# Kernel tuning notes

Hardware: AMD Instinct MI355X
Metric: run time of the kernel (lower is better)

Reference implementation:

```python
import jax, jax.numpy as jnp
import numpy as np

B, T, C = 1, 2048, 2048
H, N = 16, 128            # num_attention_heads, head_size
KVH = 4                   # num_key_value_heads
N_REP = H // KVH
D_DECAY, D_AAA, D_MV, D_MK, D_GATE = 160, 96, 64, 64, 160
ROPE_THETA = 1000000.0
EPS = 1e-6

def _rms_norm(h, w):
    var = jnp.mean(jnp.square(h.astype(jnp.float32)), axis=-1, keepdims=True)
    return (w * (h.astype(jnp.float32) * jax.lax.rsqrt(var + EPS))).astype(h.dtype)

def _rotate_half(q):
    q1, q2 = jnp.split(q, 2, axis=-1)
    return jnp.concatenate([-q2, q1], axis=-1)

def setup_inputs():
    key = jax.random.key(0)
    ks = jax.random.split(key, 24)
    f = jnp.float32
    rn = lambda k, shape, s=1.0: jax.random.normal(k, shape, dtype=f) * s
    half = N // 2
    inv_freq = 1.0 / (ROPE_THETA ** (jnp.arange(half, dtype=f) / half))
    freqs = jnp.arange(T, dtype=f)[:, None] * inv_freq[None, :]
    emb = jnp.concatenate([freqs, freqs], axis=-1)
    return {
        "x": rn(ks[0], (B, T, C)),
        "v_first": rn(ks[1], (B, T, KVH, N)),
        "k_first": rn(ks[2], (B, T, KVH, N)),
        "attention_mask": jnp.ones((B, T), f),
        "cos": jnp.cos(emb)[None],
        "sin": jnp.sin(emb)[None],
        "w0": rn(ks[3], (1, 1, H * N), 0.5) - 2.0,
        "w1": rn(ks[4], (C, D_DECAY), 0.02),
        "w2": rn(ks[5], (D_DECAY, H * N), 0.02),
        "a0": rn(ks[6], (1, 1, H * N), 0.1),
        "a1": rn(ks[7], (C, D_AAA), 0.02),
        "a2": rn(ks[8], (D_AAA, H * N), 0.02),
        "v0": rn(ks[9], (1, 1, KVH * N), 0.1) + 0.73,
        "v1": rn(ks[10], (C, D_MV), 0.02),
        "v2": rn(ks[11], (D_MV, KVH * N), 0.02),
        "k0": rn(ks[12], (1, 1, KVH * N), 0.1) + 0.73,
        "k1": rn(ks[13], (C, D_MK), 0.02),
        "k2": rn(ks[14], (D_MK, KVH * N), 0.02),
        "g1": rn(ks[15], (C, D_GATE), 0.02),
        "g2": rn(ks[16], (D_GATE, H * N), 0.02),
        "r_k": rn(ks[17], (H, N), 0.02) - 0.04,
        "r_norm_w": jnp.ones((N,), f),
        "k_norm_w": jnp.ones((N,), f),
        "W_r": rn(ks[18], (C, H * N), 0.02),
        "W_k": rn(ks[19], (C, KVH * N), 0.02),
        "W_v": rn(ks[20], (C, KVH * N), 0.02),
        "W_o": rn(ks[21], (H * N, C), 0.02),
    }

def _forward(x, v_first, k_first, attention_mask, cos, sin, w0, w1, w2, a0, a1, a2,
             v0, v1, v2, k0, k1, k2, g1, g2, r_k, r_norm_w, k_norm_w, W_r, W_k, W_v, W_o):
    xm = x * attention_mask[..., None]
    r = _rms_norm((xm @ W_r).reshape(B, T, H, N), r_norm_w)
    k = _rms_norm((xm @ W_k).reshape(B, T, KVH, N), k_norm_w)
    v = (xm @ W_v).reshape(B, T, KVH, N)
    c, s = cos[:, :, None, :], sin[:, :, None, :]   # rope, unsqueeze_dim=2
    r = r * c + _rotate_half(r) * s
    k = k * c + _rotate_half(k) * s
    w = -jax.nn.softplus(-(w0 + jnp.tanh(xm @ w1) @ w2)) - 0.5   # (B,T,H*N), always <= -0.5
    a = jax.nn.sigmoid(a0 + (xm @ a1) @ a2).reshape(B, T, H, N)  # in-context learning rate
    g = jax.nn.sigmoid(xm @ g1) @ g2                             # output gate (B,T,H*N)
    # residual mixing with first-layer value/key (layer_id > 0 branch)
    v = v + (v_first - v) * jax.nn.sigmoid(v0 + (xm @ v1) @ v2).reshape(B, T, KVH, N)
    k = k + (k_first - k) * jax.nn.sigmoid(k0 + (xm @ k1) @ k2).reshape(B, T, KVH, N)
    k = jnp.repeat(k, N_REP, axis=2)   # GQA repeat_kv -> (B,T,H,N)
    v = jnp.repeat(v, N_REP, axis=2)
    kk = k / jnp.maximum(jnp.linalg.norm(k, axis=-1, keepdims=True), 1e-12)  # F.normalize
    aa, bb = -kk, kk * a               # rank-1 state-update vectors
    wdec = jnp.exp(-jnp.exp(w.reshape(B, T, H, N)))  # per-channel decay in (0,1)

    def step(S, xs):                   # RWKV-7 state recurrence; S: (B,H,N,N) value x key
        wt, rt, kt, vt, at, bt = xs    # each (B,H,N)
        sa = jnp.einsum('bhij,bhj->bhi', S, at)
        S = S * wt[:, :, None, :] + sa[..., None] * bt[:, :, None, :] + vt[..., None] * kt[:, :, None, :]
        return S, jnp.einsum('bhij,bhj->bhi', S, rt)

    S0 = jnp.zeros((B, H, N, N), jnp.float32)
    xs = tuple(jnp.moveaxis(t, 1, 0) for t in (wdec, r, k, v, aa, bb))  # time-major
    _, y = jax.lax.scan(step, S0, xs)
    y = jnp.moveaxis(y, 0, 1)          # (B,T,H,N)
    y = y + jnp.sum(r * k * r_k, axis=-1, keepdims=True) * v   # r_k bonus term
    return (y.reshape(B, T, H * N) * g) @ W_o

def reference(x, v_first, k_first, attention_mask, cos, sin, w0, w1, w2, a0, a1, a2,
              v0, v1, v2, k0, k1, k2, g1, g2, r_k, r_norm_w, k_norm_w, W_r, W_k, W_v, W_o):
    return _forward(x, v_first, k_first, attention_mask, cos, sin, w0, w1, w2, a0, a1, a2,
                    v0, v1, v2, k0, k1, k2, g1, g2, r_k, r_norm_w, k_norm_w, W_r, W_k, W_v, W_o)
```

## Files before the change

### kernel.cpp

```cpp
#include <hip/hip_runtime.h>
#include <hip/hip_bf16.h>
#include <math.h>

#define T_   2048
#define C_   2048
#define H_   16
#define N_   128
#define KVH_ 4

typedef __bf16 bf16x8 __attribute__((ext_vector_type(8)));
typedef __bf16 bf16x4 __attribute__((ext_vector_type(4)));
typedef float  f32x4  __attribute__((ext_vector_type(4)));

#define MFMA16(a, b, c) __builtin_amdgcn_mfma_f32_16x16x32_bf16(a, b, c, 0, 0, 0)

static __device__ __forceinline__ void gll16(const __bf16* g, __bf16* l) {
    __builtin_amdgcn_global_load_lds((const __attribute__((address_space(1))) void*)g,
                                     (__attribute__((address_space(3))) void*)l, 16, 0, 0);
}

static __device__ __forceinline__ float wave_sum_shfl(float v) {
#pragma unroll
    for (int m = 32; m >= 1; m >>= 1) v += __shfl_xor(v, m, 64);
    return v;
}
static __device__ __forceinline__ float block_sum_128(float v, float* sh2) {
    v = wave_sum_shfl(v);
    if ((threadIdx.x & 63) == 0) sh2[threadIdx.x >> 6] = v;
    __syncthreads();
    float r = sh2[0] + sh2[1];
    __syncthreads();
    return r;
}

__global__ void xm_to_bf16(const float* __restrict__ x, const float* __restrict__ mask,
                           __bf16* __restrict__ o) {
    int idx = blockIdx.x * 256 + threadIdx.x;
    int e = idx * 4;
    float4 v = *(const float4*)(x + e);
    float m = mask[e >> 11];
    bf16x4 r;
    r.x = (__bf16)(v.x * m); r.y = (__bf16)(v.y * m);
    r.z = (__bf16)(v.z * m); r.w = (__bf16)(v.w * m);
    *(bf16x4*)(o + e) = r;
}

struct TrDesc { const float* src; __bf16* dst; int R, C, tileStart; };
struct TrBatch { TrDesc d[13]; int n; };

__global__ void transpose_batch(TrBatch tb) {
    int bid = blockIdx.x;
    int e = 0;
    while (e + 1 < tb.n && tb.d[e + 1].tileStart <= bid) e++;
    const float* src = tb.d[e].src;
    __bf16* dst = tb.d[e].dst;
    int R = tb.d[e].R, C = tb.d[e].C;
    int tix = bid - tb.d[e].tileStart;
    int tilesC = (C + 31) >> 5;
    int trow = tix / tilesC, tcol = tix - trow * tilesC;
    int r0 = trow * 32, c0 = tcol * 32;
    __shared__ float tile[32][33];
    int tx = threadIdx.x & 31, ty = threadIdx.x >> 5;
#pragma unroll
    for (int i = 0; i < 4; i++) {
        int r = r0 + ty + i * 8, c = c0 + tx;
        if (r < R && c < C) tile[ty + i * 8][tx] = src[(size_t)r * C + c];
    }
    __syncthreads();
#pragma unroll
    for (int i = 0; i < 4; i++) {
        int c = c0 + ty + i * 8, r = r0 + tx;
        if (c < C && r < R) dst[(size_t)c * R + r] = (__bf16)tile[tx][ty + i * 8];
    }
}

__global__ void transpose_f32_bf16(const float* __restrict__ src, __bf16* __restrict__ dst,
                                   int R, int C) {
    __shared__ float tile[32][33];
    int tx = threadIdx.x & 31, ty = threadIdx.x >> 5;
    int c0 = blockIdx.x * 32, r0 = blockIdx.y * 32;
#pragma unroll
    for (int i = 0; i < 4; i++) {
        int r = r0 + ty + i * 8, c = c0 + tx;
        if (r < R && c < C) tile[ty + i * 8][tx] = src[(size_t)r * C + c];
    }
    __syncthreads();
#pragma unroll
    for (int i = 0; i < 4; i++) {
        int c = c0 + ty + i * 8, r = r0 + tx;
        if (c < C && r < R) dst[(size_t)c * R + r] = (__bf16)tile[tx][ty + i * 8];
    }
}

template <int MODE>
__global__ __launch_bounds__(256, 2)
void gemm_bf16(const __bf16* __restrict__ A, int lda, const __bf16* __restrict__ BT,
               const float* __restrict__ bias, float* __restrict__ Cf,
               __bf16* __restrict__ Cb, int N, int K, int act) {
    __shared__ __align__(16) __bf16 As[128 * 32];
    __shared__ __align__(16) __bf16 Bs[128 * 32];
    const int tid = threadIdx.x;
    const int lane = tid & 63, wave = tid >> 6;
    const int bm = blockIdx.y * 128, bn = blockIdx.x * 128;
    const int wm = (wave >> 1) * 64, wn = (wave & 1) * 64;
    const int prow = lane >> 2, pk = (lane & 3) * 8;
    const __bf16* ApA = A + (size_t)(bm + wave * 32 + prow) * lda + pk;
    const __bf16* BpA = BT + (size_t)(bn + wave * 32 + prow) * K + pk;
    const bool bokA = (bn + wave * 32 + prow) < N;
    const bool bokB = (bn + wave * 32 + 16 + prow) < N;
    __bf16* AsD = As + wave * 1024;
    __bf16* BsD = Bs + wave * 1024;
    const int lm = lane & 15, lq = lane >> 4;
    f32x4 acc[4][4] = {};
    for (int k0 = 0; k0 < K; k0 += 32) {
        __syncthreads();
        gll16(ApA + k0, AsD);
        gll16(ApA + (size_t)16 * lda + k0, AsD + 512);
        if (bokA) gll16(BpA + k0, BsD);
        if (bokB) gll16(BpA + (size_t)16 * K + k0, BsD + 512);
        __syncthreads();
        bf16x8 af[4], bfr[4];
#pragma unroll
        for (int i = 0; i < 4; i++)
            af[i] = *(const bf16x8*)(As + (wm + i * 16 + lm) * 32 + lq * 8);
#pragma unroll
        for (int j = 0; j < 4; j++)
            bfr[j] = *(const bf16x8*)(Bs + (wn + j * 16 + lm) * 32 + lq * 8);
#pragma unroll
        for (int i = 0; i < 4; i++)
#pragma unroll
            for (int j = 0; j < 4; j++)
                acc[i][j] = MFMA16(af[i], bfr[j], acc[i][j]);
    }
#pragma unroll
    for (int j = 0; j < 4; j++) {
        int col = bn + wn + j * 16 + lm;
        if (col >= N) continue;
        float bv = (MODE == 0 && bias) ? bias[col] : 0.f;
#pragma unroll
        for (int i = 0; i < 4; i++) {
            int row0 = bm + wm + i * 16 + lq * 4;
#pragma unroll
            for (int rg = 0; rg < 4; rg++) {
                float v = acc[i][j][rg] + bv;
                int row = row0 + rg;
                if (MODE == 0) {
                    if (act == 1) v = tanhf(v);
                    else if (act == 2) v = 1.f / (1.f + __expf(-v));
                    Cf[(size_t)row * N + col] = v;
                } else {
                    if (col < 3072) {
                        Cf[(size_t)row * 3072 + col] = v;
                    } else {
                        float vv = v;
                        if (col < 3232) vv = tanhf(v);
                        else if (col >= 3456) vv = 1.f / (1.f + __expf(-v));
                        Cb[(size_t)row * 544 + (col - 3072)] = (__bf16)vv;
                    }
                }
            }
        }
    }
}

struct GSeg { const __bf16* BT; const float* bias; float* Cf; int aoff, K, N, act, bx0; };
struct GB5 { GSeg s[5]; };

__global__ __launch_bounds__(256, 2)
void gemm_group(const __bf16* __restrict__ Abase, GB5 gb) {
    __shared__ __align__(16) __bf16 As[128 * 32];
    __shared__ __align__(16) __bf16 Bs[128 * 32];
    int e = 0;
    while (e + 1 < 5 && gb.s[e + 1].bx0 <= (int)blockIdx.x) e++;
    const GSeg sg = gb.s[e];
    const int K = sg.K, N = sg.N;
    const __bf16* A = Abase + sg.aoff;
    const int tid = threadIdx.x;
    const int lane = tid & 63, wave = tid >> 6;
    const int bm = blockIdx.y * 128, bn = (blockIdx.x - sg.bx0) * 128;
    const int wm = (wave >> 1) * 64, wn = (wave & 1) * 64;
    const int prow = lane >> 2, pk = (lane & 3) * 8;
    const __bf16* ApA = A + (size_t)(bm + wave * 32 + prow) * 544 + pk;
    const __bf16* BpA = sg.BT + (size_t)(bn + wave * 32 + prow) * K + pk;
    __bf16* AsD = As + wave * 1024;
    __bf16* BsD = Bs + wave * 1024;
    const int lm = lane & 15, lq = lane >> 4;
    f32x4 acc[4][4] = {};
    for (int k0 = 0; k0 < K; k0 += 32) {
        __syncthreads();
        gll16(ApA + k0, AsD);
        gll16(ApA + (size_t)16 * 544 + k0, AsD + 512);
        gll16(BpA + k0, BsD);
        gll16(BpA + (size_t)16 * K + k0, BsD + 512);
        __syncthreads();
        bf16x8 af[4], bfr[4];
#pragma unroll
        for (int i = 0; i < 4; i++)
            af[i] = *(const bf16x8*)(As + (wm + i * 16 + lm) * 32 + lq * 8);
#pragma unroll
        for (int j = 0; j < 4; j++)
            bfr[j] = *(const bf16x8*)(Bs + (wn + j * 16 + lm) * 32 + lq * 8);
#pragma unroll
        for (int i = 0; i < 4; i++)
#pragma unroll
            for (int j = 0; j < 4; j++)
                acc[i][j] = MFMA16(af[i], bfr[j], acc[i][j]);
    }
#pragma unroll
    for (int j = 0; j < 4; j++) {
        int col = bn + wn + j * 16 + lm;
        float bv = sg.bias ? sg.bias[col] : 0.f;
#pragma unroll
        for (int i = 0; i < 4; i++) {
            int row0 = bm + wm + i * 16 + lq * 4;
#pragma unroll
            for (int rg = 0; rg < 4; rg++) {
                float v = acc[i][j][rg] + bv;
                if (sg.act == 2) v = 1.f / (1.f + __expf(-v));
                sg.Cf[(size_t)(row0 + rg) * N + col] = v;
            }
        }
    }
}

__global__ __launch_bounds__(128)
void prep_kv(float* __restrict__ mega, float* __restrict__ kkO,
             const float* __restrict__ kfirst, const float* __restrict__ vfirst,
             const float* __restrict__ kmix, const float* __restrict__ vmix,
             const float* __restrict__ cosT, const float* __restrict__ sinT,
             const float* __restrict__ knw) {
    __shared__ float sh[128];
    __shared__ float sh2[2];
    int b = blockIdx.x;
    int t = b >> 2, kvh = b & 3;
    int n = threadIdx.x;
    size_t kbase = (size_t)t * 3072 + 2048 + kvh * 128;
    size_t vbase = (size_t)t * 3072 + 2560 + kvh * 128;
    size_t fbase = (size_t)t * 512 + kvh * 128;
    float x = mega[kbase + n];
    float ssq = block_sum_128(x * x, sh2);
    float kn = knw[n] * (x * rsqrtf(ssq * (1.f / 128.f) + 1e-6f));
    sh[n] = kn;
    __syncthreads();
    float rot = (n < 64) ? -sh[n + 64] : sh[n - 64];
    float c = cosT[(size_t)t * 128 + n], s = sinT[(size_t)t * 128 + n];
    float kr = kn * c + rot * s;
    float kf = kr + (kfirst[fbase + n] - kr) * kmix[fbase + n];
    float s2 = block_sum_128(kf * kf, sh2);
    float kkv = kf / fmaxf(sqrtf(s2), 1e-12f);
    float vv = mega[vbase + n];
    float vf = vv + (vfirst[fbase + n] - vv) * vmix[fbase + n];
    mega[kbase + n] = kf;
    kkO[fbase + n] = kkv;
    mega[vbase + n] = vf;
}

__global__ __launch_bounds__(128)
void prep_r(float* __restrict__ mega, float* __restrict__ Wl,
            const float* __restrict__ rk, float* __restrict__ cOut,
            const float* __restrict__ cosT, const float* __restrict__ sinT,
            const float* __restrict__ rnw) {
    __shared__ float sh[128];
    __shared__ float sh2[2];
    int b = blockIdx.x;
    int t = b >> 4, h = b & 15;
    int kv = h >> 2;
    int n = threadIdx.x;
    size_t rbase = (size_t)t * 3072 + h * 128;
    float x = mega[rbase + n];
    float ssq = block_sum_128(x * x, sh2);
    float rn = rnw[n] * (x * rsqrtf(ssq * (1.f / 128.f) + 1e-6f));
    sh[n] = rn;
    __syncthreads();
    float rot = (n < 64) ? -sh[n + 64] : sh[n - 64];
    float c = cosT[(size_t)t * 128 + n], s = sinT[(size_t)t * 128 + n];
    float rr = rn * c + rot * s;
    mega[rbase + n] = rr;
    size_t wb_ = (size_t)t * 2048 + h * 128 + n;
    float z = Wl[wb_];
    float nz = -z;
    float sp = fmaxf(nz, 0.f) + log1pf(expf(-fabsf(nz)));
    float w = -sp - 0.5f;
    Wl[wb_] = expf(-expf(w));
    float pc = rr * mega[(size_t)t * 3072 + 2048 + kv * 128 + n] * rk[h * 128 + n];
    float cs = block_sum_128(pc, sh2);
    if (n == 0) cOut[b] = cs;
}


__global__ __launch_bounds__(64)
void scan_phaseA(const float* __restrict__ Wl, const float* __restrict__ megaF,
                 const float* __restrict__ aS, const float* __restrict__ kkB,
                 __bf16* __restrict__ ATt_g, __bf16* __restrict__ Rr_g,
                 __bf16* __restrict__ Bnt_g, __bf16* __restrict__ Knt_g,
                 __bf16* __restrict__ Vt_g, __bf16* __restrict__ Gbt_g,
                 __bf16* __restrict__ Gkt_g, float* __restrict__ Cloc_g,
                 float* __restrict__ cwL_g) {
    __shared__ __align__(16) __bf16 pool[27648];
    __bf16* Arm = pool;
    __bf16* Brm = pool + 4352;
    __bf16* Krm = pool + 8704;
    __bf16* Rrm = pool + 13056;
    __bf16* Vt  = pool + 17408;
    __bf16* Mrm = pool + 22528;
    __bf16* Mt  = pool + 23808;
    __bf16* Prm = pool + 25088;
    __bf16* Gtmp= pool + 26368;
    __bf16* M2rm = pool + 4352;
    __bf16* M2t  = pool + 5632;
    __bf16* Xa   = pool + 6912;
    __bf16* Xb   = pool + 8192;
    __bf16* Tt   = pool + 9472;
    __bf16* PTt  = pool + 10752;
    __bf16* Ant  = pool + 13056;

    const int l = threadIdx.x, lm = l & 15, lq = l >> 4;
    const int u = blockIdx.x, h = u >> 6, c = u & 63, kv = h >> 2;
    const int n0 = l, n1 = l + 64;

    float cw0 = 1.f, cw1 = 1.f;
    for (int t = 0; t < 32; ++t) {
        int tg = c * 32 + t;
        size_t hb = (size_t)tg * 2048 + h * 128;
        size_t mb = (size_t)tg * 3072;
        size_t kb = (size_t)tg * 512 + kv * 128;
        float wv0 = Wl[hb + n0], wv1 = Wl[hb + n1];
        float r0 = megaF[mb + h * 128 + n0], r1 = megaF[mb + h * 128 + n1];
        float q0 = kkB[kb + n0], q1 = kkB[kb + n1];
        float s0 = aS[hb + n0], s1 = aS[hb + n1];
        float k0 = megaF[mb + 2048 + kv * 128 + n0], k1 = megaF[mb + 2048 + kv * 128 + n1];
        float v0 = megaF[mb + 2560 + kv * 128 + n0], v1 = megaF[mb + 2560 + kv * 128 + n1];
        float cp0 = cw0, cp1 = cw1;
        cw0 *= wv0; cw1 *= wv1;
        float ic0 = 1.f / cw0, ic1 = 1.f / cw1;
        Arm[t * 136 + n0] = (__bf16)(-cp0 * q0);
        Arm[t * 136 + n1] = (__bf16)(-cp1 * q1);
        Brm[t * 136 + n0] = (__bf16)(q0 * s0 * ic0);
        Brm[t * 136 + n1] = (__bf16)(q1 * s1 * ic1);
        Krm[t * 136 + n0] = (__bf16)(k0 * ic0);
        Krm[t * 136 + n1] = (__bf16)(k1 * ic1);
        Rrm[t * 136 + n0] = (__bf16)(cw0 * r0);
        Rrm[t * 136 + n1] = (__bf16)(cw1 * r1);
        Vt[n0 * 40 + t] = (__bf16)v0;
        Vt[n1 * 40 + t] = (__bf16)v1;
    }
    cwL_g[(size_t)u * 128 + n0] = cw0;
    cwL_g[(size_t)u * 128 + n1] = cw1;

    auto mmLL = [&](const __bf16* Ao, const __bf16* Bo, bool incl, __bf16* dTr, __bf16* dDir) {
#pragma unroll
        for (int ri = 0; ri < 2; ri++)
#pragma unroll
        for (int ci = 0; ci < 2; ci++) {
            f32x4 acc = {};
#pragma unroll
            for (int s = 0; s < 4; s++) {
                bf16x8 af = *(const bf16x8*)(Ao + (ri * 16 + lm) * 136 + s * 32 + lq * 8);
                bf16x8 bf = *(const bf16x8*)(Bo + (ci * 16 + lm) * 136 + s * 32 + lq * 8);
                acc = MFMA16(af, bf, acc);
            }
#pragma unroll
            for (int rg = 0; rg < 4; rg++) {
                int rr = ri * 16 + lq * 4 + rg, cc = ci * 16 + lm;
                bool keep = incl ? (cc <= rr) : (cc < rr);
                __bf16 bv = (__bf16)(keep ? acc[rg] : 0.f);
                if (dTr)  dTr[cc * 40 + rr] = bv;
                if (dDir) dDir[rr * 40 + cc] = bv;
            }
        }
    };
    mmLL(Arm, Brm, false, Mrm, Mt);
    mmLL(Arm, Krm, false, Prm, nullptr);
    mmLL(Rrm, Brm, true, nullptr, Gtmp);
    for (int i = l; i < 512; i += 64) {
        int r = i >> 4, cp = i & 15;
        ((int*)(Gbt_g + (size_t)u * 1024))[i] = *(const int*)(Gtmp + r * 40 + cp * 2);
    }
    mmLL(Rrm, Krm, true, nullptr, Gtmp);
    for (int i = l; i < 512; i += 64) {
        int r = i >> 4, cp = i & 15;
        ((int*)(Gkt_g + (size_t)u * 1024))[i] = *(const int*)(Gtmp + r * 40 + cp * 2);
    }
    for (int i = l; i < 2048; i += 64) {
        int t = i >> 6, cp = i & 63;
        ((int*)(Rr_g + (size_t)u * 4096))[i] = *(const int*)(Rrm + t * 136 + cp * 2);
    }
    for (int i = l; i < 2048; i += 64) {
        int n = i >> 4, tp = i & 15;
        unsigned int lo = ((const unsigned short*)Brm)[(2 * tp) * 136 + n];
        unsigned int hi = ((const unsigned short*)Brm)[(2 * tp + 1) * 136 + n];
        ((unsigned int*)(Bnt_g + (size_t)u * 4096))[i] = lo | (hi << 16);
        unsigned int lo2 = ((const unsigned short*)Krm)[(2 * tp) * 136 + n];
        unsigned int hi2 = ((const unsigned short*)Krm)[(2 * tp + 1) * 136 + n];
        ((unsigned int*)(Knt_g + (size_t)u * 4096))[i] = lo2 | (hi2 << 16);
    }
    for (int i = l; i < 2048; i += 64) {
        int n = i >> 4, tp = i & 15;
        ((int*)(Vt_g + (size_t)u * 4096))[i] = *(const int*)(Vt + n * 40 + tp * 2);
    }

    for (int i = l; i < 1024; i += 64) {
        int s = i >> 5, t = i & 31;
        Xa[s * 40 + t] = (s == t) ? (__bf16)1.f : Mrm[s * 40 + t];
    }
    for (int i = l; i < 4096; i += 64) {
        int s = i & 31, n = i >> 5;
        Ant[n * 32 + s] = Arm[s * 136 + n];
    }

    auto mat32 = [&](const __bf16* Ao, const __bf16* Bo, const __bf16* accIn,
                     __bf16* oRm, __bf16* oT) {
#pragma unroll
        for (int ri = 0; ri < 2; ri++)
#pragma unroll
        for (int ci = 0; ci < 2; ci++) {
            f32x4 acc = {};
            if (accIn) {
#pragma unroll
                for (int rg = 0; rg < 4; rg++)
                    acc[rg] = (float)accIn[(ri * 16 + lq * 4 + rg) * 40 + ci * 16 + lm];
            }
            bf16x8 af = *(const bf16x8*)(Ao + (ri * 16 + lm) * 40 + lq * 8);
            bf16x8 bf = *(const bf16x8*)(Bo + (ci * 16 + lm) * 40 + lq * 8);
            acc = MFMA16(af, bf, acc);
#pragma unroll
            for (int rg = 0; rg < 4; rg++) {
                int rr = ri * 16 + lq * 4 + rg, cc = ci * 16 + lm;
                __bf16 bv = (__bf16)acc[rg];
                if (oRm) oRm[rr * 40 + cc] = bv;
                if (oT)  oT[cc * 40 + rr] = bv;
            }
        }
    };
    mat32(Mrm, Mt, nullptr, M2rm, M2t);
    mat32(Xa, M2t, Xa, Xb, nullptr);
    mat32(M2rm, M2t, nullptr, Mrm, Mt);
    mat32(Xb, Mt, Xb, Xa, nullptr);
    mat32(Mrm, Mt, nullptr, M2rm, M2t);
    mat32(Xa, M2t, Xa, Xb, nullptr);
    mat32(M2rm, M2t, nullptr, Mrm, Mt);
    mat32(Xb, Mt, Xb, nullptr, Tt);
    mat32(Tt, Prm, nullptr, PTt, nullptr);

#pragma unroll
    for (int ti = 0; ti < 2; ti++) {
        bf16x8 af = *(const bf16x8*)(Tt + (ti * 16 + lm) * 40 + lq * 8);
#pragma unroll
        for (int ni = 0; ni < 8; ni++) {
            f32x4 accv = {};
            bf16x8 bfv = *(const bf16x8*)(Ant + (ni * 16 + lm) * 32 + lq * 8);
            accv = MFMA16(af, bfv, accv);
#pragma unroll
            for (int rg = 0; rg < 4; rg++)
                ATt_g[(size_t)u * 4096 + (ti * 16 + lq * 4 + rg) * 128 + ni * 16 + lm] = (__bf16)accv[rg];
        }
    }
#pragma unroll
    for (int ii = 0; ii < 8; ii++)
#pragma unroll
    for (int ti = 0; ti < 2; ti++) {
        f32x4 acc = {};
        bf16x8 af = *(const bf16x8*)(Vt + (ii * 16 + lm) * 40 + lq * 8);
        bf16x8 bf = *(const bf16x8*)(PTt + (ti * 16 + lm) * 40 + lq * 8);
        acc = MFMA16(af, bf, acc);
#pragma unroll
        for (int rg = 0; rg < 4; rg++)
            Cloc_g[(size_t)u * 4096 + (ii * 16 + lq * 4 + rg) * 32 + ti * 16 + lm] = acc[rg];
    }
}

struct Ops {
    bf16x8 at[8], bn[8], kn[8], vf;
    f32x4 cl[2];
    float cw[8];
};

__global__ __launch_bounds__(64, 1)
void scan_phaseB(const __bf16* __restrict__ ATt_g, const __bf16* __restrict__ Bnt_g,
                 const __bf16* __restrict__ Knt_g, const __bf16* __restrict__ Vt_g,
                 const float* __restrict__ Cloc_g, const float* __restrict__ cwL_g,
                 __bf16* __restrict__ Sg, __bf16* __restrict__ Cg) {
    __shared__ __align__(16) __bf16 Sbf[16 * 136];
    __shared__ __align__(16) __bf16 Cbf[16 * 40];
    const int h = blockIdx.y, i0 = blockIdx.x * 16;
    const int l = threadIdx.x, lm = l & 15, lq = l >> 4;
    f32x4 st[8];
#pragma unroll
    for (int cc = 0; cc < 8; cc++) st[cc] = (f32x4){0.f, 0.f, 0.f, 0.f};

    auto loadOps = [&](int c, Ops& o) {
        size_t u = (size_t)h * 64 + c;
        const __bf16* ATp = ATt_g + u * 4096;
        const __bf16* Bp  = Bnt_g + u * 4096;
        const __bf16* Kp  = Knt_g + u * 4096;
#pragma unroll
        for (int ti = 0; ti < 2; ti++)
#pragma unroll
            for (int s = 0; s < 4; s++)
                o.at[ti * 4 + s] = *(const bf16x8*)(ATp + (ti * 16 + lm) * 128 + s * 32 + lq * 8);
#pragma unroll
        for (int cc = 0; cc < 8; cc++) {
            o.bn[cc] = *(const bf16x8*)(Bp + (cc * 16 + lm) * 32 + lq * 8);
            o.kn[cc] = *(const bf16x8*)(Kp + (cc * 16 + lm) * 32 + lq * 8);
        }
        o.vf = *(const bf16x8*)(Vt_g + u * 4096 + (size_t)(i0 + lm) * 32 + lq * 8);
#pragma unroll
        for (int ti = 0; ti < 2; ti++)
#pragma unroll
            for (int rg = 0; rg < 4; rg++)
                o.cl[ti][rg] = Cloc_g[u * 4096 + (i0 + lq * 4 + rg) * 32 + ti * 16 + lm];
#pragma unroll
        for (int cc = 0; cc < 8; cc++) o.cw[cc] = cwL_g[u * 128 + cc * 16 + lm];
    };

    auto computeChunk = [&](int c, const Ops& o) {
        size_t u = (size_t)h * 64 + c;
#pragma unroll
        for (int cc = 0; cc < 8; cc++)
#pragma unroll
            for (int rg = 0; rg < 4; rg++)
                Sbf[(lq * 4 + rg) * 136 + cc * 16 + lm] = (__bf16)st[cc][rg];
        bf16x8 saf[4];
#pragma unroll
        for (int s = 0; s < 4; s++)
            saf[s] = *(const bf16x8*)(Sbf + lm * 136 + s * 32 + lq * 8);
        f32x4 cacc[2];
#pragma unroll
        for (int ti = 0; ti < 2; ti++) {
            f32x4 acc = o.cl[ti];
#pragma unroll
            for (int s = 0; s < 4; s++) acc = MFMA16(saf[s], o.at[ti * 4 + s], acc);
            cacc[ti] = acc;
        }
#pragma unroll
        for (int ti = 0; ti < 2; ti++)
#pragma unroll
            for (int rg = 0; rg < 4; rg++)
                Cbf[(lq * 4 + rg) * 40 + ti * 16 + lm] = (__bf16)cacc[ti][rg];
        bf16x8 cf = *(const bf16x8*)(Cbf + lm * 40 + lq * 8);
#pragma unroll
        for (int s = 0; s < 4; s++)
            *(bf16x8*)(Sg + u * 16384 + (size_t)(i0 + lm) * 128 + s * 32 + lq * 8) = saf[s];
        *(bf16x8*)(Cg + u * 4096 + (size_t)(i0 + lm) * 32 + lq * 8) = cf;
#pragma unroll
        for (int cc = 0; cc < 8; cc++) {
            st[cc] = MFMA16(cf, o.bn[cc], st[cc]);
            st[cc] = MFMA16(o.vf, o.kn[cc], st[cc]);
#pragma unroll
            for (int rg = 0; rg < 4; rg++) st[cc][rg] *= o.cw[cc];
        }
    };

    Ops A, B;
    loadOps(0, A);
    loadOps(1, B);
    for (int c = 0; c < 64; c += 2) {
        computeChunk(c, A);
        if (c + 2 < 64) loadOps(c + 2, A);
        computeChunk(c + 1, B);
        if (c + 3 < 64) loadOps(c + 3, B);
    }
}

__global__ __launch_bounds__(64)
void scan_phaseC(const __bf16* __restrict__ Sg, const __bf16* __restrict__ Cg,
                 const __bf16* __restrict__ Rr_g, const __bf16* __restrict__ Vt_g,
                 const __bf16* __restrict__ Gbt_g, const __bf16* __restrict__ Gkt_g,
                 const float* __restrict__ cB, const float* __restrict__ megaF,
                 const float* __restrict__ gB, __bf16* __restrict__ out) {
    __shared__ float Ybuf[32 * 18];
    const int bx = blockIdx.x, h = blockIdx.y;
    const int c = bx >> 3, i0 = (bx & 7) * 16;
    const int l = threadIdx.x, lm = l & 15, lq = l >> 4;
    const size_t u = (size_t)h * 64 + c;
    bf16x8 saf[4];
#pragma unroll
    for (int s = 0; s < 4; s++)
        saf[s] = *(const bf16x8*)(Sg + u * 16384 + (size_t)(i0 + lm) * 128 + s * 32 + lq * 8);
    bf16x8 cf = *(const bf16x8*)(Cg + u * 4096 + (size_t)(i0 + lm) * 32 + lq * 8);
    bf16x8 vf = *(const bf16x8*)(Vt_g + u * 4096 + (size_t)(i0 + lm) * 32 + lq * 8);
#pragma unroll
    for (int ti = 0; ti < 2; ti++) {
        f32x4 acc = {};
#pragma unroll
        for (int s = 0; s < 4; s++) {
            bf16x8 rp = *(const bf16x8*)(Rr_g + u * 4096 + (ti * 16 + lm) * 128 + s * 32 + lq * 8);
            acc = MFMA16(saf[s], rp, acc);
        }
        bf16x8 gb = *(const bf16x8*)(Gbt_g + u * 1024 + (ti * 16 + lm) * 32 + lq * 8);
        acc = MFMA16(cf, gb, acc);
        bf16x8 gk = *(const bf16x8*)(Gkt_g + u * 1024 + (ti * 16 + lm) * 32 + lq * 8);
        acc = MFMA16(vf, gk, acc);
#pragma unroll
        for (int rg = 0; rg < 4; rg++)
            Ybuf[(ti * 16 + lm) * 18 + lq * 4 + rg] = acc[rg];
    }
    const int kv = h >> 2;
#pragma unroll
    for (int pass = 0; pass < 8; pass++) {
        int t = pass * 4 + lq;
        int tg = c * 32 + t;
        int col = h * 128 + i0 + lm;
        float yv = Ybuf[t * 18 + lm];
        float cv = cB[tg * 16 + h];
        float vv = megaF[(size_t)tg * 3072 + 2560 + kv * 128 + i0 + lm];
        float gg = gB[(size_t)tg * 2048 + col];
        out[(size_t)tg * 2048 + col] = (__bf16)((yv + cv * vv) * gg);
    }
}

extern "C" void kernel_launch(void* const* d_in, const int* in_sizes, int n_in,
                              void* d_out, int out_size, void* d_ws, size_t ws_size,
                              hipStream_t stream) {
    (void)in_sizes; (void)n_in; (void)out_size; (void)ws_size;
    const float* x      = (const float*)d_in[0];
    const float* vfirst = (const float*)d_in[1];
    const float* kfirst = (const float*)d_in[2];
    const float* amask  = (const float*)d_in[3];
    const float* cosT   = (const float*)d_in[4];
    const float* sinT   = (const float*)d_in[5];
    const float* w0     = (const float*)d_in[6];
    const float* w1     = (const float*)d_in[7];
    const float* w2     = (const float*)d_in[8];
    const float* a0     = (const float*)d_in[9];
    const float* a1     = (const float*)d_in[10];
    const float* a2     = (const float*)d_in[11];
    const float* v0     = (const float*)d_in[12];
    const float* v1     = (const float*)d_in[13];
    const float* v2     = (const float*)d_in[14];
    const float* k0     = (const float*)d_in[15];
    const float* k1     = (const float*)d_in[16];
    const float* k2     = (const float*)d_in[17];
    const float* g1     = (const float*)d_in[18];
    const float* g2     = (const float*)d_in[19];
    const float* rk     = (const float*)d_in[20];
    const float* rnw    = (const float*)d_in[21];
    const float* knw    = (const float*)d_in[22];
    const float* W_r    = (const float*)d_in[23];
    const float* W_k    = (const float*)d_in[24];
    const float* W_v    = (const float*)d_in[25];
    const float* W_o    = (const float*)d_in[26];

    char* p = (char*)d_ws;
    auto take = [&](size_t bytes) { char* r = p; p += (bytes + 255) & ~(size_t)255; return r; };
    __bf16* arena   = (__bf16*)take((size_t)3616 * 2048 * 2);
    __bf16* xmb     = (__bf16*)take((size_t)T_ * C_ * 2);
    float*  megaF   = (float*)take((size_t)T_ * 3072 * 4);
    __bf16* megaB   = (__bf16*)take((size_t)T_ * 544 * 2);
    __bf16* w2T     = (__bf16*)take((size_t)2048 * 160 * 2);
    __bf16* a2T     = (__bf16*)take((size_t)2048 * 96 * 2);
    __bf16* v2T     = (__bf16*)take((size_t)512 * 64 * 2);
    __bf16* k2T     = (__bf16*)take((size_t)512 * 64 * 2);
    __bf16* g2T     = (__bf16*)take((size_t)2048 * 160 * 2);
    float*  Wl      = (float*)take((size_t)T_ * 2048 * 4);
    float*  aS      = (float*)take((size_t)T_ * 2048 * 4);
    float*  gB      = (float*)take((size_t)T_ * 2048 * 4);
    float*  kkB     = (float*)take((size_t)T_ * 512 * 4);
    float*  vmx     = (float*)take((size_t)T_ * 512 * 4);
    float*  kmx     = (float*)take((size_t)T_ * 512 * 4);
    float*  cB      = (float*)take((size_t)T_ * H_ * 4);
    __bf16* ATt_g   = (__bf16*)take((size_t)1024 * 4096 * 2);
    __bf16* Rr_g    = (__bf16*)take((size_t)1024 * 4096 * 2);
    __bf16* Bnt_g   = (__bf16*)take((size_t)1024 * 4096 * 2);
    __bf16* Knt_g   = (__bf16*)take((size_t)1024 * 4096 * 2);
    __bf16* Vt_g    = (__bf16*)take((size_t)1024 * 4096 * 2);
    __bf16* Gbt_g   = (__bf16*)take((size_t)1024 * 1024 * 2);
    __bf16* Gkt_g   = (__bf16*)take((size_t)1024 * 1024 * 2);
    float*  Cloc_g  = (float*)take((size_t)1024 * 4096 * 4);
    float*  cwL_g   = (float*)take((size_t)1024 * 128 * 4);
    __bf16* Sg = (__bf16*)Wl;
    __bf16* Cg = (__bf16*)kkB;

    xm_to_bf16<<<(T_ * C_ / 4) / 256, 256, 0, stream>>>(x, amask, xmb);

    TrBatch tb;
    {
        const float* srcs[13] = {W_r, W_k, W_v, w1, a1, v1, k1, g1, w2, a2, v2, k2, g2};
        __bf16* dsts[13] = {arena, arena + (size_t)2048 * 2048, arena + (size_t)2560 * 2048,
                            arena + (size_t)3072 * 2048, arena + (size_t)3232 * 2048,
                            arena + (size_t)3328 * 2048, arena + (size_t)3392 * 2048,
                            arena + (size_t)3456 * 2048, w2T, a2T, v2T, k2T, g2T};
        int Rs[13] = {2048, 2048, 2048, 2048, 2048, 2048, 2048, 2048, 160, 96, 64, 64, 160};
        int Cs[13] = {2048, 512, 512, 160, 96, 64, 64, 160, 2048, 2048, 512, 512, 2048};
        int cum = 0;
        for (int e = 0; e < 13; e++) {
            tb.d[e].src = srcs[e]; tb.d[e].dst = dsts[e];
            tb.d[e].R = Rs[e]; tb.d[e].C = Cs[e]; tb.d[e].tileStart = cum;
            cum += ((Rs[e] + 31) / 32) * ((Cs[e] + 31) / 32);
        }
        tb.n = 13;
        transpose_batch<<<cum, 256, 0, stream>>>(tb);
    }

    gemm_bf16<2><<<dim3(29, 16), 256, 0, stream>>>(xmb, 2048, arena, nullptr, megaF, megaB, 3616, 2048, 0);

    GB5 gb;
    gb.s[0] = {w2T, w0, Wl,  0,   160, 2048, 0, 0};
    gb.s[1] = {a2T, a0, aS,  160, 96,  2048, 2, 16};
    gb.s[2] = {v2T, v0, vmx, 256, 64,  512,  2, 32};
    gb.s[3] = {k2T, k0, kmx, 320, 64,  512,  2, 36};
    gb.s[4] = {g2T, nullptr, gB, 384, 160, 2048, 0, 40};
    gemm_group<<<dim3(56, 16), 256, 0, stream>>>(megaB, gb);

    prep_kv<<<T_ * KVH_, 128, 0, stream>>>(megaF, kkB, kfirst, vfirst, kmx, vmx, cosT, sinT, knw);
    prep_r<<<T_ * H_, 128, 0, stream>>>(megaF, Wl, rk, cB, cosT, sinT, rnw);

    scan_phaseA<<<1024, 64, 0, stream>>>(Wl, megaF, aS, kkB, ATt_g, Rr_g, Bnt_g, Knt_g,
                                         Vt_g, Gbt_g, Gkt_g, Cloc_g, cwL_g);
    scan_phaseB<<<dim3(8, 16), 64, 0, stream>>>(ATt_g, Bnt_g, Knt_g, Vt_g, Cloc_g, cwL_g, Sg, Cg);
    scan_phaseC<<<dim3(512, 16), 64, 0, stream>>>(Sg, Cg, Rr_g, Vt_g, Gbt_g, Gkt_g,
                                                  cB, megaF, gB, xmb);

    transpose_f32_bf16<<<dim3(64, 64), 256, 0, stream>>>(W_o, arena, 2048, 2048);
    gemm_bf16<0><<<dim3(16, 16), 256, 0, stream>>>(xmb, 2048, arena, nullptr, (float*)d_out, nullptr, 2048, 2048, 0);
}
```

Measured before the change: 519.0 us.

## Store scan operands in MFMA-fragment order and triple-buffer phase-B chunk loads

Phase A now writes ATt, Bnt, Knt, Vt and Cloc in the exact per-lane fragment order that phase B's MFMAs consume. Phase B can then fetch each operand with contiguous 16-byte per-lane loads instead of strided gathers. The sequential scan loop also moves from two to three operand buffers, so global loads have more time to complete before they are used. The cost is more registers in a kernel limited to one wave per block, and every consumer of these buffers, including phase C's Vt read, must agree on the new layout.

Result: faster. 496.4 us (-4.4%).

```diff
diff --git a/kernel.cpp b/kernel.cpp
--- a/kernel.cpp
+++ b/kernel.cpp
@@ -387,16 +387,14 @@
     }
     for (int i = l; i < 2048; i += 64) {
         int n = i >> 4, tp = i & 15;
+        int idx = (n >> 4) * 256 + (tp >> 2) * 64 + (n & 15) * 4 + (tp & 3);
         unsigned int lo = ((const unsigned short*)Brm)[(2 * tp) * 136 + n];
         unsigned int hi = ((const unsigned short*)Brm)[(2 * tp + 1) * 136 + n];
-        ((unsigned int*)(Bnt_g + (size_t)u * 4096))[i] = lo | (hi << 16);
+        ((unsigned int*)(Bnt_g + (size_t)u * 4096))[idx] = lo | (hi << 16);
         unsigned int lo2 = ((const unsigned short*)Krm)[(2 * tp) * 136 + n];
         unsigned int hi2 = ((const unsigned short*)Krm)[(2 * tp + 1) * 136 + n];
-        ((unsigned int*)(Knt_g + (size_t)u * 4096))[i] = lo2 | (hi2 << 16);
-    }
-    for (int i = l; i < 2048; i += 64) {
-        int n = i >> 4, tp = i & 15;
-        ((int*)(Vt_g + (size_t)u * 4096))[i] = *(const int*)(Vt + n * 40 + tp * 2);
+        ((unsigned int*)(Knt_g + (size_t)u * 4096))[idx] = lo2 | (hi2 << 16);
+        ((unsigned int*)(Vt_g + (size_t)u * 4096))[idx] = *(const unsigned int*)(Vt + n * 40 + tp * 2);
     }
 
     for (int i = l; i < 1024; i += 64) {
@@ -451,8 +449,11 @@
             bf16x8 bfv = *(const bf16x8*)(Ant + (ni * 16 + lm) * 32 + lq * 8);
             accv = MFMA16(af, bfv, accv);
 #pragma unroll
-            for (int rg = 0; rg < 4; rg++)
-                ATt_g[(size_t)u * 4096 + (ti * 16 + lq * 4 + rg) * 128 + ni * 16 + lm] = (__bf16)accv[rg];
+            for (int rg = 0; rg < 4; rg++) {
+                int off = (ti * 4 + (ni >> 1)) * 512 + ((ni & 1) * 2 + (lm >> 3)) * 128
+                        + (lq * 4 + rg) * 8 + (lm & 7);
+                ATt_g[(size_t)u * 4096 + off] = (__bf16)accv[rg];
+            }
         }
     }
 #pragma unroll
@@ -463,9 +464,7 @@
         bf16x8 af = *(const bf16x8*)(Vt + (ii * 16 + lm) * 40 + lq * 8);
         bf16x8 bf = *(const bf16x8*)(PTt + (ti * 16 + lm) * 40 + lq * 8);
         acc = MFMA16(af, bf, acc);
-#pragma unroll
-        for (int rg = 0; rg < 4; rg++)
-            Cloc_g[(size_t)u * 4096 + (ii * 16 + lq * 4 + rg) * 32 + ti * 16 + lm] = acc[rg];
+        *(f32x4*)(Cloc_g + (size_t)u * 4096 + ii * 512 + ti * 256 + l * 4) = acc;
     }
 }
 
@@ -490,25 +489,19 @@
 
     auto loadOps = [&](int c, Ops& o) {
         size_t u = (size_t)h * 64 + c;
-        const __bf16* ATp = ATt_g + u * 4096;
-        const __bf16* Bp  = Bnt_g + u * 4096;
-        const __bf16* Kp  = Knt_g + u * 4096;
-#pragma unroll
-        for (int ti = 0; ti < 2; ti++)
-#pragma unroll
-            for (int s = 0; s < 4; s++)
-                o.at[ti * 4 + s] = *(const bf16x8*)(ATp + (ti * 16 + lm) * 128 + s * 32 + lq * 8);
-#pragma unroll
-        for (int cc = 0; cc < 8; cc++) {
-            o.bn[cc] = *(const bf16x8*)(Bp + (cc * 16 + lm) * 32 + lq * 8);
-            o.kn[cc] = *(const bf16x8*)(Kp + (cc * 16 + lm) * 32 + lq * 8);
-        }
-        o.vf = *(const bf16x8*)(Vt_g + u * 4096 + (size_t)(i0 + lm) * 32 + lq * 8);
-#pragma unroll
-        for (int ti = 0; ti < 2; ti++)
-#pragma unroll
-            for (int rg = 0; rg < 4; rg++)
-                o.cl[ti][rg] = Cloc_g[u * 4096 + (i0 + lq * 4 + rg) * 32 + ti * 16 + lm];
+        const __bf16* ab = ATt_g + u * 4096 + (size_t)l * 8;
+        const __bf16* bb = Bnt_g + u * 4096 + (size_t)l * 8;
+        const __bf16* kb = Knt_g + u * 4096 + (size_t)l * 8;
+#pragma unroll
+        for (int j = 0; j < 8; j++) {
+            o.at[j] = *(const bf16x8*)(ab + j * 512);
+            o.bn[j] = *(const bf16x8*)(bb + j * 512);
+            o.kn[j] = *(const bf16x8*)(kb + j * 512);
+        }
+        o.vf = *(const bf16x8*)(Vt_g + u * 4096 + (i0 >> 4) * 512 + (size_t)l * 8);
+        const float* clb = Cloc_g + u * 4096 + (i0 >> 4) * 512 + (size_t)l * 4;
+        o.cl[0] = *(const f32x4*)(clb);
+        o.cl[1] = *(const f32x4*)(clb + 256);
 #pragma unroll
         for (int cc = 0; cc < 8; cc++) o.cw[cc] = cwL_g[u * 128 + cc * 16 + lm];
     };
@@ -551,15 +544,20 @@
         }
     };
 
-    Ops A, B;
+    Ops A, B, C;
     loadOps(0, A);
     loadOps(1, B);
-    for (int c = 0; c < 64; c += 2) {
+    loadOps(2, C);
+    int c = 0;
+    for (; c + 2 < 64; c += 3) {
         computeChunk(c, A);
-        if (c + 2 < 64) loadOps(c + 2, A);
+        if (c + 3 < 64) loadOps(c + 3, A);
         computeChunk(c + 1, B);
-        if (c + 3 < 64) loadOps(c + 3, B);
-    }
+        if (c + 4 < 64) loadOps(c + 4, B);
+        computeChunk(c + 2, C);
+        if (c + 5 < 64) loadOps(c + 5, C);
+    }
+    computeChunk(63, A);
 }
 
 __global__ __launch_bounds__(64)
@@ -578,7 +576,7 @@
     for (int s = 0; s < 4; s++)
         saf[s] = *(const bf16x8*)(Sg + u * 16384 + (size_t)(i0 + lm) * 128 + s * 32 + lq * 8);
     bf16x8 cf = *(const bf16x8*)(Cg + u * 4096 + (size_t)(i0 + lm) * 32 + lq * 8);
-    bf16x8 vf = *(const bf16x8*)(Vt_g + u * 4096 + (size_t)(i0 + lm) * 32 + lq * 8);
+    bf16x8 vf = *(const bf16x8*)(Vt_g + u * 4096 + (i0 >> 4) * 512 + (size_t)l * 8);
 #pragma unroll
     for (int ti = 0; ti < 2; ti++) {
         f32x4 acc = {};
```
